# Performance work log

Hardware: AMD Instinct MI355X
Metric: run time of the kernel (lower is better)

Reference implementation:

```python
import jax, jax.numpy as jnp
import numpy as np

B, T = 8, 4096
H, V, K = 512, 32000, 9


def setup_inputs() -> dict:
    key = jax.random.key(0)
    k1, k2, k3 = jax.random.split(key, 3)
    x = jax.random.randint(k1, (B, T), 0, V, dtype=jnp.int32)
    # conv1d weight [out_ch=H, in_ch=V, K], xavier-like scale
    scale = 1.0 / np.sqrt(V * K)
    W = jax.random.normal(k2, (H, V, K), dtype=jnp.float32) * scale
    b = jax.random.normal(k3, (H,), dtype=jnp.float32) * 0.01
    return {"x": x, "W": W, "b": b}


def reference(x, W, b):
    """one_hot(x, V) -> conv1d(V->H, K, pad=K//2) expressed as gather+sum.

    out[b,t,c] = bias[c] + sum_k W[c, x[b, t+k-pad], k]  (zero outside [0,T)).
    """
    Bx, Tx = x.shape
    Hh, Vv, Kk = W.shape
    pad = Kk // 2
    t = jnp.arange(Tx)
    acc = jnp.zeros((Bx, Tx, Hh), dtype=W.dtype)
    for k in range(Kk):  # small fixed kernel loop (K=9)
        src = t + (k - pad)                      # [T]
        valid = (src >= 0) & (src < Tx)          # [T]
        src_c = jnp.clip(src, 0, Tx - 1)
        ids = x[:, src_c]                        # [B,T]
        emb = jnp.take(W[:, :, k].T, ids, axis=0)  # [B,T,H] gather of column k
        acc = acc + jnp.where(valid[None, :, None], emb, jnp.zeros((), W.dtype))
    return acc + b  # [B,T,H]
```

## Files before the change

### kernel.cpp

```cpp
#include <hip/hip_runtime.h>
#include <hip/hip_bf16.h>


#define Hc 512
#define Vc 32000
#define Kc 9
#define Tc 4096
#define Bc 8
#define Mc (Vc * Kc)
#define CHUNK_C 128
#define NCHUNK 4
#define ROW_U (Kc * CHUNK_C / 2)
#define WT_ROWS (Vc + 1)
#define T_TILE 32

__device__ __forceinline__ unsigned int f2bf(float f) {
  unsigned int u = __float_as_uint(f);
  u += 0x7FFFu + ((u >> 16) & 1u);
  return u >> 16;
}

__global__ __launch_bounds__(256) void mark_kernel(
    const int* __restrict__ x, int* __restrict__ slot, int* __restrict__ counter) {
  const int i = blockIdx.x * 256 + threadIdx.x;
  const int v = x[i];
  if (atomicCAS(&slot[v], -1, -2147483647) == -1) {
    slot[v] = 1 + atomicAdd(counter, 1);
  }
}

__global__ __launch_bounds__(256) void transpose_chunk_kernel(
    const float* __restrict__ W, const int* __restrict__ slot,
    unsigned int* __restrict__ wbuf, int chunk) {
  __shared__ float tile[64][65];
  const int m0 = blockIdx.x * 64;
  const int ct = blockIdx.y;
  const int cbase = chunk * CHUNK_C + ct * 64;
  const int tid = threadIdx.x;
  const int tx = tid & 63;
  const int ty = tid >> 6;
#pragma unroll
  for (int r = 0; r < 16; ++r) {
    const int row = ty * 16 + r;
    tile[row][tx] = W[(size_t)(cbase + row) * Mc + (m0 + tx)];
  }
  __syncthreads();
  const int u = tid & 31;
  const int rl = tid >> 5;
#pragma unroll
  for (int p = 0; p < 8; ++p) {
    const int mrow = p * 8 + rl;
    const int m = m0 + mrow;
    const int v = m / Kc;
    const int k = m - v * Kc;
    const int s = slot[v];
    if (s >= 0) {
      const unsigned int val = f2bf(tile[2 * u][mrow]) |
                               (f2bf(tile[2 * u + 1][mrow]) << 16);
      wbuf[(size_t)s * ROW_U + k * (CHUNK_C / 2) + ct * 32 + u] = val;
    }
  }
}

__global__ __launch_bounds__(256) void gather_chunk_kernel(
    const int* __restrict__ x, const int* __restrict__ slot,
    const unsigned int* __restrict__ rbuf, const float* __restrict__ bias,
    float* __restrict__ out, int chunk) {
  __shared__ int ids[T_TILE + Kc - 1];
  const int gb = blockIdx.x;
  const int b = gb >> 7;
  const int t0 = (gb & 127) * T_TILE;
  const int tid = threadIdx.x;
  if (tid < T_TILE + Kc - 1) {
    const int s = t0 + tid - (Kc / 2);
    ids[tid] = (s >= 0 && s < Tc) ? slot[x[b * Tc + s]] : 0;
  }
  __syncthreads();
  const int lane = tid & 63;
  const int w = tid >> 6;
  const int c0 = chunk * CHUNK_C;
  const int cpl = 2 * lane;
  const float2 b2 = *(const float2*)(bias + c0 + cpl);
#pragma unroll
  for (int i = 0; i < 8; ++i) {
    const int tt = w * 8 + i;
    float2 acc = b2;
#pragma unroll
    for (int k = 0; k < Kc; ++k) {
      const int id = ids[tt + k];
      const unsigned int wv =
          rbuf[(size_t)id * ROW_U + k * (CHUNK_C / 2) + lane];
      acc.x += __uint_as_float(wv << 16);
      acc.y += __uint_as_float(wv & 0xFFFF0000u);
    }
    *(float2*)(out + ((size_t)(b * Tc + t0 + tt) << 9) + c0 + cpl) = acc;
  }
}

__global__ __launch_bounds__(256) void conv_fallback_kernel(
    const int* __restrict__ x, const float* __restrict__ W,
    const float* __restrict__ bias, float* __restrict__ out) {
  const size_t idx = (size_t)blockIdx.x * 256 + threadIdx.x;
  const int c = (int)(idx & (Hc - 1));
  const size_t bt = idx >> 9;
  const int t = (int)(bt & (Tc - 1));
  const int b = (int)(bt >> 12);
  float acc = bias[c];
#pragma unroll
  for (int k = 0; k < Kc; ++k) {
    const int s = t + k - (Kc / 2);
    if (s >= 0 && s < Tc) {
      const int id = x[b * Tc + s];
      acc += W[(size_t)c * Mc + (size_t)id * Kc + k];
    }
  }
  out[idx] = acc;
}

extern "C" void kernel_launch(void* const* d_in, const int* in_sizes, int n_in,
                              void* d_out, int out_size, void* d_ws, size_t ws_size,
                              hipStream_t stream) {
  const int* x = (const int*)d_in[0];
  const float* W = (const float*)d_in[1];
  const float* bias = (const float*)d_in[2];
  float* out = (float*)d_out;

  const size_t buf_bytes = (size_t)WT_ROWS * ROW_U * 4;
  const size_t slot_off = buf_bytes;
  const size_t cnt_off = slot_off + (size_t)Vc * 4;
  const size_t need = cnt_off + 4;

  if (ws_size >= need) {
    unsigned int* buf = (unsigned int*)d_ws;
    int* slot = (int*)((char*)d_ws + slot_off);
    int* counter = (int*)((char*)d_ws + cnt_off);
    hipMemsetAsync(slot, 0xFF, (size_t)Vc * 4, stream);
    hipMemsetAsync(counter, 0, 4, stream);
    hipMemsetAsync(buf, 0, ROW_U * 4, stream);
    mark_kernel<<<(Bc * Tc) / 256, 256, 0, stream>>>(x, slot, counter);
    dim3 tg(4500, 2);
    for (int chunk = 0; chunk < NCHUNK; ++chunk) {
      transpose_chunk_kernel<<<tg, 256, 0, stream>>>(W, slot, buf, chunk);
      gather_chunk_kernel<<<1024, 256, 0, stream>>>(x, slot, buf, bias, out,
                                                    chunk);
    }
  } else {
    const size_t n = (size_t)Bc * Tc * Hc;
    conv_fallback_kernel<<<(int)(n / 256), 256, 0, stream>>>(x, W, bias, out);
  }
}
```

Baseline: 241.0 us.

## Halve channel chunk, widen loads, and vectorize gather with nontemporal stores

Splits the channel dimension into 8 chunks of 64 instead of 4 of 128, which halves the bf16 staging buffer per chunk so it is more likely to stay cache-resident. The transpose kernel now reads W as 8-byte nontemporal loads over a 128-column tile. The gather kernel uses 64-timestep tiles and 16-byte vector loads and nontemporal float4 stores for the output. The cost is twice as many kernel launches and twice as many passes over the token ids.

```diff
diff --git a/kernel.cpp b/kernel.cpp
--- a/kernel.cpp
+++ b/kernel.cpp
@@ -1,5 +1,4 @@
 #include <hip/hip_runtime.h>
-#include <hip/hip_bf16.h>
 
 
 #define Hc 512
@@ -8,11 +7,14 @@
 #define Tc 4096
 #define Bc 8
 #define Mc (Vc * Kc)
-#define CHUNK_C 128
-#define NCHUNK 4
+#define CHUNK_C 64
+#define NCHUNK 8
 #define ROW_U (Kc * CHUNK_C / 2)
 #define WT_ROWS (Vc + 1)
-#define T_TILE 32
+#define MT 128
+#define T_TILE 64
+
+typedef float f4v __attribute__((ext_vector_type(4)));
 
 __device__ __forceinline__ unsigned int f2bf(float f) {
   unsigned int u = __float_as_uint(f);
@@ -32,32 +34,36 @@
 __global__ __launch_bounds__(256) void transpose_chunk_kernel(
     const float* __restrict__ W, const int* __restrict__ slot,
     unsigned int* __restrict__ wbuf, int chunk) {
-  __shared__ float tile[64][65];
-  const int m0 = blockIdx.x * 64;
-  const int ct = blockIdx.y;
-  const int cbase = chunk * CHUNK_C + ct * 64;
+  __shared__ float tile[MT][CHUNK_C + 1];
+  const int m0 = blockIdx.x * MT;
+  const int cbase = chunk * CHUNK_C;
   const int tid = threadIdx.x;
   const int tx = tid & 63;
   const int ty = tid >> 6;
 #pragma unroll
-  for (int r = 0; r < 16; ++r) {
-    const int row = ty * 16 + r;
-    tile[row][tx] = W[(size_t)(cbase + row) * Mc + (m0 + tx)];
+  for (int i = 0; i < 16; ++i) {
+    const int cr = i * 4 + ty;
+    const double* p =
+        (const double*)(W + (size_t)(cbase + cr) * Mc + m0) + tx;
+    const double d = __builtin_nontemporal_load(p);
+    const float2 f = *(const float2*)&d;
+    tile[2 * tx][cr] = f.x;
+    tile[2 * tx + 1][cr] = f.y;
   }
   __syncthreads();
   const int u = tid & 31;
   const int rl = tid >> 5;
 #pragma unroll
-  for (int p = 0; p < 8; ++p) {
-    const int mrow = p * 8 + rl;
-    const int m = m0 + mrow;
+  for (int p = 0; p < 16; ++p) {
+    const int mr = p * 8 + rl;
+    const int m = m0 + mr;
     const int v = m / Kc;
     const int k = m - v * Kc;
     const int s = slot[v];
     if (s >= 0) {
-      const unsigned int val = f2bf(tile[2 * u][mrow]) |
-                               (f2bf(tile[2 * u + 1][mrow]) << 16);
-      wbuf[(size_t)s * ROW_U + k * (CHUNK_C / 2) + ct * 32 + u] = val;
+      const unsigned int val =
+          f2bf(tile[mr][2 * u]) | (f2bf(tile[mr][2 * u + 1]) << 16);
+      wbuf[(size_t)s * ROW_U + k * 32 + u] = val;
     }
   }
 }
@@ -68,32 +74,34 @@
     float* __restrict__ out, int chunk) {
   __shared__ int ids[T_TILE + Kc - 1];
   const int gb = blockIdx.x;
-  const int b = gb >> 7;
-  const int t0 = (gb & 127) * T_TILE;
+  const int b = gb >> 6;
+  const int t0 = (gb & 63) * T_TILE;
   const int tid = threadIdx.x;
   if (tid < T_TILE + Kc - 1) {
     const int s = t0 + tid - (Kc / 2);
     ids[tid] = (s >= 0 && s < Tc) ? slot[x[b * Tc + s]] : 0;
   }
   __syncthreads();
-  const int lane = tid & 63;
-  const int w = tid >> 6;
+  const int cq = tid & 15;
+  const int r = tid >> 4;
   const int c0 = chunk * CHUNK_C;
-  const int cpl = 2 * lane;
-  const float2 b2 = *(const float2*)(bias + c0 + cpl);
+  const f4v b4 = *(const f4v*)(bias + c0 + 4 * cq);
+  const uint2* rb2 = (const uint2*)rbuf;
 #pragma unroll
-  for (int i = 0; i < 8; ++i) {
-    const int tt = w * 8 + i;
-    float2 acc = b2;
+  for (int i = 0; i < 4; ++i) {
+    const int tt = r * 4 + i;
+    f4v acc = b4;
 #pragma unroll
     for (int k = 0; k < Kc; ++k) {
       const int id = ids[tt + k];
-      const unsigned int wv =
-          rbuf[(size_t)id * ROW_U + k * (CHUNK_C / 2) + lane];
-      acc.x += __uint_as_float(wv << 16);
-      acc.y += __uint_as_float(wv & 0xFFFF0000u);
+      const uint2 wv = rb2[(size_t)id * (ROW_U / 2) + k * 16 + cq];
+      acc.x += __uint_as_float(wv.x << 16);
+      acc.y += __uint_as_float(wv.x & 0xFFFF0000u);
+      acc.z += __uint_as_float(wv.y << 16);
+      acc.w += __uint_as_float(wv.y & 0xFFFF0000u);
     }
-    *(float2*)(out + ((size_t)(b * Tc + t0 + tt) << 9) + c0 + cpl) = acc;
+    __builtin_nontemporal_store(
+        acc, (f4v*)(out + ((size_t)(b * Tc + t0 + tt) << 9) + c0 + 4 * cq));
   }
 }
 
@@ -138,11 +146,10 @@
     hipMemsetAsync(counter, 0, 4, stream);
     hipMemsetAsync(buf, 0, ROW_U * 4, stream);
     mark_kernel<<<(Bc * Tc) / 256, 256, 0, stream>>>(x, slot, counter);
-    dim3 tg(4500, 2);
     for (int chunk = 0; chunk < NCHUNK; ++chunk) {
-      transpose_chunk_kernel<<<tg, 256, 0, stream>>>(W, slot, buf, chunk);
-      gather_chunk_kernel<<<1024, 256, 0, stream>>>(x, slot, buf, bias, out,
-                                                    chunk);
+      transpose_chunk_kernel<<<Mc / MT, 256, 0, stream>>>(W, slot, buf, chunk);
+      gather_chunk_kernel<<<Bc * (Tc / T_TILE), 256, 0, stream>>>(
+          x, slot, buf, bias, out, chunk);
     }
   } else {
     const size_t n = (size_t)Bc * Tc * Hc;
```

Result: slower. 301.1 us (+24.9%).
